# Performance work log

Hardware: AMD Instinct MI355X
Metric: run time of the kernel (lower is better)

The kernel has to match this reference:

```python
import jax, jax.numpy as jnp
import numpy as np
from jax.ops import segment_sum

N = 100000
E = 3200000
IN_DIM = 256
OUT_DIM = 64
LN_EPS = 1e-5
NEG_SLOPE = 0.01


def setup_inputs() -> dict:
    key = jax.random.key(0)
    k1, k2, k3, k4, k5 = jax.random.split(key, 5)
    x = jax.random.normal(k1, (N, IN_DIM), dtype=jnp.float32)
    edge_index = jax.random.randint(k2, (2, E), 0, N, dtype=jnp.int32)
    edge_weight = jax.random.uniform(k3, (E,), dtype=jnp.float32)
    # GCNConv params (glorot-ish scale) + LayerNorm params
    W = jax.random.normal(k4, (IN_DIM, OUT_DIM), dtype=jnp.float32) / np.sqrt(IN_DIM)
    b = jnp.zeros((OUT_DIM,), dtype=jnp.float32)
    gamma = jnp.ones((OUT_DIM,), dtype=jnp.float32)
    beta = jnp.zeros((OUT_DIM,), dtype=jnp.float32)
    return {"x": x, "edge_index": edge_index, "edge_weight": edge_weight,
            "W": W, "b": b, "gamma": gamma, "beta": beta}


def _gcn_forward(x, edge_index, edge_weight, W, b, gamma, beta):
    n = x.shape[0]
    # add self-loops with weight 1 (PyG GCNConv default)
    loops = jnp.arange(n, dtype=edge_index.dtype)
    src = jnp.concatenate([edge_index[0], loops])   # [E+N] message sources
    dst = jnp.concatenate([edge_index[1], loops])   # [E+N] aggregation targets
    ew = jnp.concatenate([edge_weight, jnp.ones((n,), dtype=edge_weight.dtype)])
    # symmetric normalization: deg computed on dst via weighted scatter
    deg = segment_sum(ew, dst, num_segments=n)                   # [N]
    dinv = jnp.where(deg > 0, jax.lax.rsqrt(deg), 0.0)           # deg^{-1/2}
    norm = dinv[src] * ew * dinv[dst]                            # [E+N]
    h = x @ W                                                    # [N, OUT]
    agg = segment_sum(h[src] * norm[:, None], dst, num_segments=n)  # [N, OUT]
    y = agg + b
    # leaky_relu then LayerNorm over last dim
    y = jnp.where(y >= 0, y, NEG_SLOPE * y)
    mu = jnp.mean(y, axis=-1, keepdims=True)
    var = jnp.mean(jnp.square(y - mu), axis=-1, keepdims=True)
    return (y - mu) * jax.lax.rsqrt(var + LN_EPS) * gamma + beta


def reference(x, edge_index, edge_weight, W, b, gamma, beta):
    return _gcn_forward(x, edge_index, edge_weight, W, b, gamma, beta)
```

## Files before the change

kernel.cpp:

```cpp
#include <hip/hip_runtime.h>

#define NN 100000
#define NE 3200000
#define OVCAP 65536

#define BINSZ 64
#define NBIN ((NN + BINSZ - 1) / BINSZ)
#define MAXPB 4096
#define SCAT_BLOCKS 512

struct OvEnt { int dst; int src; float ew; int pad; };


__global__ void k_zero(int* __restrict__ bincnt, int* __restrict__ ovcnt, int n) {
    int i = blockIdx.x * 256 + threadIdx.x;
    if (i < n) bincnt[i] = 0;
    if (i == 0) *ovcnt = 0;
}

__global__ __launch_bounds__(256) void k_binscatter(
    const int* __restrict__ src, const int* __restrict__ dst,
    const float* __restrict__ ew, int* __restrict__ bincnt,
    uint2* __restrict__ binbuf, int cap,
    OvEnt* __restrict__ ov, int* __restrict__ ovcnt, int e) {
    __shared__ int hist[NBIN];
    int t = threadIdx.x;
    int chunk = (e + gridDim.x - 1) / gridDim.x;
    int beg = blockIdx.x * chunk;
    int end = beg + chunk; if (end > e) end = e;
    for (int j = t; j < NBIN; j += 256) hist[j] = 0;
    __syncthreads();
    for (int i = beg + t; i < end; i += 256)
        atomicAdd(&hist[dst[i] >> 6], 1);
    __syncthreads();
    for (int j = t; j < NBIN; j += 256) {
        int c = hist[j];
        hist[j] = (c > 0) ? atomicAdd(&bincnt[j], c) : 0;
    }
    __syncthreads();
    for (int i = beg + t; i < end; i += 256) {
        int s = src[i], d = dst[i];
        float w = ew[i];
        int bin = d >> 6;
        int pos = atomicAdd(&hist[bin], 1);
        if (pos < cap) {
            unsigned key = (unsigned)s | ((unsigned)(d & 63) << 17);
            binbuf[(size_t)bin * cap + pos] = make_uint2(key, __float_as_uint(w));
        } else {
            int op = atomicAdd(ovcnt, 1);
            if (op < OVCAP) { OvEnt t2; t2.dst = d; t2.src = s; t2.ew = w; t2.pad = 0; ov[op] = t2; }
        }
    }
}

__global__ __launch_bounds__(256) void k_binsort(
    const int* __restrict__ bincnt, uint2* __restrict__ binbuf, int cap,
    const OvEnt* __restrict__ ov, const int* __restrict__ ovcnt,
    float* __restrict__ dinv, int* __restrict__ off, int* __restrict__ ncnt,
    int* __restrict__ binov, int n) {
    __shared__ float sdeg[BINSZ];
    __shared__ int hcnt[BINSZ];
    __shared__ int hoff[BINSZ];
    __shared__ int sov;
    __shared__ uint2 sbuf[MAXPB];
    int bin = blockIdx.x, t = threadIdx.x;
    if (t < BINSZ) { sdeg[t] = 0.f; hcnt[t] = 0; }
    if (t == 0) {
        int c = bincnt[bin];
        sov = (c > cap);
        binov[bin] = (c > cap);
    }
    __syncthreads();
    int cnt = bincnt[bin];
    int bc = cnt < cap ? cnt : cap;
    uint2* base = binbuf + (size_t)bin * cap;
    uint2 ent[16];
    int ne = 0;
#pragma unroll
    for (int p = 0; p < 16; p++) {
        int idx = t + p * 256;
        if (idx < bc) { ent[p] = base[idx]; ne = p + 1; }
    }
#pragma unroll
    for (int p = 0; p < 16; p++) {
        if (p < ne) {
            int dl = (int)((ent[p].x >> 17) & 63u);
            atomicAdd(&hcnt[dl], 1);
            atomicAdd(&sdeg[dl], __uint_as_float(ent[p].y));
        }
    }
    if (sov) {
        int on = *ovcnt; if (on > OVCAP) on = OVCAP;
        for (int j = t; j < on; j += 256) {
            OvEnt e2 = ov[j];
            if ((e2.dst >> 6) == bin) atomicAdd(&sdeg[e2.dst & 63], e2.ew);
        }
    }
    __syncthreads();
    if (t < 64) {
        int v = hcnt[t];
        int inc = v;
#pragma unroll
        for (int o2 = 1; o2 < 64; o2 <<= 1) {
            int u = __shfl_up(inc, o2, 64);
            if (t >= o2) inc += u;
        }
        int excl = inc - v;
        hoff[t] = excl;
        int g = bin * BINSZ + t;
        if (g < n) {
            dinv[g] = rsqrtf(1.0f + sdeg[t]);
            off[g] = bin * cap + excl;
            ncnt[g] = v;
        }
    }
    __syncthreads();
#pragma unroll
    for (int p = 0; p < 16; p++) {
        if (p < ne) {
            int dl = (int)((ent[p].x >> 17) & 63u);
            int pos = atomicAdd(&hoff[dl], 1);
            sbuf[pos] = ent[p];
        }
    }
    __syncthreads();
    for (int j = t; j < bc; j += 256) base[j] = sbuf[j];
}

__global__ __launch_bounds__(256) void k_norm(
    uint2* __restrict__ binbuf, const int* __restrict__ bincnt, int cap,
    const float* __restrict__ dinv, int n) {
    __shared__ float sd[BINSZ];
    int bin = blockIdx.x, t = threadIdx.x;
    if (t < BINSZ) {
        int g = bin * BINSZ + t;
        sd[t] = (g < n) ? dinv[g] : 0.f;
    }
    __syncthreads();
    int cnt = bincnt[bin];
    int bc = cnt < cap ? cnt : cap;
    uint2* base = binbuf + (size_t)bin * cap;
    for (int i = t; i < bc; i += 256) {
        uint2 v = base[i];
        int s = (int)(v.x & 0x1FFFFu);
        int dl = (int)((v.x >> 17) & 63u);
        float w = __uint_as_float(v.y) * dinv[s] * sd[dl];
        base[i] = make_uint2(v.x, __float_as_uint(w));
    }
}

__global__ __launch_bounds__(256) void k_gather_s(
    const float* __restrict__ h, const float* __restrict__ dinv,
    const int* __restrict__ binov,
    const int* __restrict__ off, const int* __restrict__ ncnt,
    const uint2* __restrict__ sorted,
    const OvEnt* __restrict__ ov, const int* __restrict__ ovcnt,
    const float* __restrict__ bias, const float* __restrict__ gamma,
    const float* __restrict__ beta, float* __restrict__ out, int n) {
    int lane = threadIdx.x & 63, wid = threadIdx.x >> 6;
    int node = blockIdx.x * 4 + wid;
    if (node >= n) return;
    float di = dinv[node];
    float acc = h[(size_t)node * 64 + lane] * di * di;
    int beg = off[node], c0 = ncnt[node];
    for (int j = 0; j < c0; j += 64) {
        int c = c0 - j; if (c > 64) c = 64;
        int s = 0; float w = 0.f;
        if (lane < c) {
            uint2 v = sorted[beg + j + lane];
            s = (int)(v.x & 0x1FFFFu);
            w = __uint_as_float(v.y);
        }
        int i2 = 0;
        for (; i2 + 16 <= c; i2 += 16) {
            float hv[16], wv[16];
#pragma unroll
            for (int q = 0; q < 16; q++) {
                int si = __shfl(s, i2 + q, 64);
                wv[q] = __shfl(w, i2 + q, 64);
                hv[q] = h[(size_t)si * 64 + lane];
            }
#pragma unroll
            for (int q = 0; q < 16; q++) acc += hv[q] * wv[q];
        }
        if (i2 < c) {
            float hv[16], wv[16];
            int rem = c - i2;
#pragma unroll
            for (int q = 0; q < 16; q++) {
                if (q < rem) {
                    int si = __shfl(s, i2 + q, 64);
                    wv[q] = __shfl(w, i2 + q, 64);
                    hv[q] = h[(size_t)si * 64 + lane];
                } else { wv[q] = 0.f; hv[q] = 0.f; }
            }
#pragma unroll
            for (int q = 0; q < 16; q++) acc += hv[q] * wv[q];
        }
    }
    if (binov[node >> 6]) {
        int on = *ovcnt; if (on > OVCAP) on = OVCAP;
        for (int j = 0; j < on; j++) {
            OvEnt ent = ov[j];
            if (ent.dst == node)
                acc += h[(size_t)ent.src * 64 + lane] * dinv[ent.src] * ent.ew * di;
        }
    }
    float y = acc + bias[lane];
    y = (y >= 0.f) ? y : 0.01f * y;
    float sum = y;
#pragma unroll
    for (int o = 32; o > 0; o >>= 1) sum += __shfl_xor(sum, o, 64);
    float mu = sum * (1.0f / 64.0f);
    float d = y - mu;
    float v = d * d;
#pragma unroll
    for (int o = 32; o > 0; o >>= 1) v += __shfl_xor(v, o, 64);
    v *= (1.0f / 64.0f);
    out[(size_t)node * 64 + lane] = d * rsqrtf(v + 1e-5f) * gamma[lane] + beta[lane];
}

#define GR 64
#define GKC 32
#define XS_STRIDE 36
__global__ __launch_bounds__(256) void k_gemm(const float* __restrict__ x,
                                              const float* __restrict__ W,
                                              float* __restrict__ h, int n) {
    __shared__ float xs[GR][XS_STRIDE];
    __shared__ float wsh[GKC][64];
    int t = threadIdx.x;
    int tx = t & 15;
    int ty = t >> 4;
    int rbase = blockIdx.x * GR;
    float acc[4][4];
#pragma unroll
    for (int i = 0; i < 4; i++)
#pragma unroll
        for (int j = 0; j < 4; j++) acc[i][j] = 0.0f;

    for (int k0 = 0; k0 < 256; k0 += GKC) {
        const float4* wsrc = (const float4*)(W + k0 * 64);
        float4* wdst = (float4*)(&wsh[0][0]);
        wdst[t] = wsrc[t];
        wdst[t + 256] = wsrc[t + 256];
#pragma unroll
        for (int p = 0; p < 2; p++) {
            int f4 = p * 256 + t;
            int r = f4 >> 3;
            int kq = (f4 & 7) << 2;
            int row = rbase + r;
            float4 val = make_float4(0.f, 0.f, 0.f, 0.f);
            if (row < n) val = *(const float4*)(x + (size_t)row * 256 + k0 + kq);
            *(float4*)(&xs[r][kq]) = val;
        }
        __syncthreads();
        int r0 = ty * 4, c0 = tx * 4;
#pragma unroll
        for (int kk = 0; kk < GKC; kk += 4) {
            float4 wv[4];
#pragma unroll
            for (int m = 0; m < 4; m++) wv[m] = *(const float4*)(&wsh[kk + m][c0]);
#pragma unroll
            for (int i = 0; i < 4; i++) {
                float4 xv = *(const float4*)(&xs[r0 + i][kk]);
                acc[i][0] += xv.x * wv[0].x + xv.y * wv[1].x + xv.z * wv[2].x + xv.w * wv[3].x;
                acc[i][1] += xv.x * wv[0].y + xv.y * wv[1].y + xv.z * wv[2].y + xv.w * wv[3].y;
                acc[i][2] += xv.x * wv[0].z + xv.y * wv[1].z + xv.z * wv[2].z + xv.w * wv[3].z;
                acc[i][3] += xv.x * wv[0].w + xv.y * wv[1].w + xv.z * wv[2].w + xv.w * wv[3].w;
            }
        }
        __syncthreads();
    }
    int r0 = ty * 4, c0 = tx * 4;
#pragma unroll
    for (int i = 0; i < 4; i++) {
        int row = rbase + r0 + i;
        if (row < n) {
            float4 v = make_float4(acc[i][0], acc[i][1], acc[i][2], acc[i][3]);
            *(float4*)(h + (size_t)row * 64 + c0) = v;
        }
    }
}


__global__ void k_init(float* __restrict__ deg, int* __restrict__ cnt, int n) {
    int i = blockIdx.x * 256 + threadIdx.x;
    if (i < n) { deg[i] = 1.0f; cnt[i] = 0; }
}

__global__ void k_deg(const int* __restrict__ dst, const float* __restrict__ ew,
                      float* __restrict__ deg, int* __restrict__ cnt, int e) {
    int i = blockIdx.x * 256 + threadIdx.x;
    if (i < e) {
        int d = dst[i];
        atomicAdd(&deg[d], ew[i]);
        atomicAdd(&cnt[d], 1);
    }
}

#define SCAN_T 256
#define SCAN_E 8
__global__ void k_scan_blocks(const int* __restrict__ cnt, int* __restrict__ off,
                              int* __restrict__ bsum, int n) {
    __shared__ int sdata[SCAN_T];
    int base = blockIdx.x * (SCAN_T * SCAN_E);
    int t = threadIdx.x;
    int v[SCAN_E];
    int local = 0;
    int idx0 = base + t * SCAN_E;
#pragma unroll
    for (int i = 0; i < SCAN_E; i++) {
        int idx = idx0 + i;
        int c = (idx < n) ? cnt[idx] : 0;
        v[i] = local;
        local += c;
    }
    sdata[t] = local;
    __syncthreads();
    for (int o = 1; o < SCAN_T; o <<= 1) {
        int x = 0;
        if (t >= o) x = sdata[t - o];
        __syncthreads();
        sdata[t] += x;
        __syncthreads();
    }
    int excl = sdata[t] - local;
#pragma unroll
    for (int i = 0; i < SCAN_E; i++) {
        int idx = idx0 + i;
        if (idx < n) off[idx] = excl + v[i];
    }
    if (t == SCAN_T - 1) bsum[blockIdx.x] = sdata[t];
}

__global__ void k_scan_bsums(int* __restrict__ bsum, int nb) {
    int t = threadIdx.x;
    int v = (t < nb) ? bsum[t] : 0;
    int orig = v;
#pragma unroll
    for (int o = 1; o < 64; o <<= 1) {
        int u = __shfl_up(v, o, 64);
        if (t >= o) v += u;
    }
    if (t < nb) bsum[t] = v - orig;
}

__global__ void k_finalize(int* __restrict__ off, const int* __restrict__ bsum,
                           int* __restrict__ cursor, float* __restrict__ deg,
                           int n, int total) {
    int i = blockIdx.x * 256 + threadIdx.x;
    if (i < n) {
        int o = off[i] + bsum[i >> 11];
        off[i] = o;
        cursor[i] = o;
        deg[i] = rsqrtf(deg[i]);
    }
    if (i == 0) off[n] = total;
}

__global__ void k_scatter(const int* __restrict__ src, const int* __restrict__ dst,
                          const float* __restrict__ ew, const float* __restrict__ dinv,
                          int* __restrict__ cursor, int* __restrict__ ssrc,
                          float* __restrict__ snorm, int e) {
    int i = blockIdx.x * 256 + threadIdx.x;
    if (i < e) {
        int s = src[i], d = dst[i];
        float nm = dinv[s] * ew[i] * dinv[d];
        int pos = atomicAdd(&cursor[d], 1);
        ssrc[pos] = s;
        snorm[pos] = nm;
    }
}

__global__ __launch_bounds__(256) void k_gather(
    const float* __restrict__ h, const float* __restrict__ dinv,
    const int* __restrict__ off, const int* __restrict__ ssrc,
    const float* __restrict__ snorm, const float* __restrict__ bias,
    const float* __restrict__ gamma, const float* __restrict__ beta,
    float* __restrict__ out, int n) {
    int lane = threadIdx.x & 63;
    int wid = threadIdx.x >> 6;
    int node = blockIdx.x * 4 + wid;
    if (node >= n) return;
    float di = dinv[node];
    float acc = h[(size_t)node * 64 + lane] * di * di;
    int beg = off[node], end = off[node + 1];
    for (int j = beg; j < end; j += 64) {
        int cnt = end - j;
        if (cnt > 64) cnt = 64;
        int s = 0;
        float w = 0.f;
        if (lane < cnt) { s = ssrc[j + lane]; w = snorm[j + lane]; }
        for (int i2 = 0; i2 < cnt; i2++) {
            int si = __shfl(s, i2, 64);
            float wi = __shfl(w, i2, 64);
            acc += h[(size_t)si * 64 + lane] * wi;
        }
    }
    float y = acc + bias[lane];
    y = (y >= 0.f) ? y : 0.01f * y;
    float sum = y;
#pragma unroll
    for (int o = 32; o > 0; o >>= 1) sum += __shfl_xor(sum, o, 64);
    float mu = sum * (1.0f / 64.0f);
    float d = y - mu;
    float v = d * d;
#pragma unroll
    for (int o = 32; o > 0; o >>= 1) v += __shfl_xor(v, o, 64);
    v *= (1.0f / 64.0f);
    out[(size_t)node * 64 + lane] = d * rsqrtf(v + 1e-5f) * gamma[lane] + beta[lane];
}


extern "C" void kernel_launch(void* const* d_in, const int* in_sizes, int n_in,
                              void* d_out, int out_size, void* d_ws, size_t ws_size,
                              hipStream_t stream) {
    const float* x = (const float*)d_in[0];
    const int* ei = (const int*)d_in[1];
    const float* ew = (const float*)d_in[2];
    const float* W = (const float*)d_in[3];
    const float* b = (const float*)d_in[4];
    const float* gamma = (const float*)d_in[5];
    const float* beta = (const float*)d_in[6];
    float* out = (float*)d_out;

    const int n = NN, e = NE;
    const int* src = ei;
    const int* dst = ei + e;

    char* ws = (char*)d_ws;
    size_t o = 0;
    auto alloc = [&](size_t bytes) -> char* {
        char* r = ws + o;
        o = (o + bytes + 255) & ~(size_t)255;
        return r;
    };
    auto pad = [](size_t bytes) -> size_t { return (bytes + 255) & ~(size_t)255; };

    int nb_n = (n + 255) / 256;
    int nb_e = (e + 255) / 256;
    int nb_gemm = (n + GR - 1) / GR;
    int nb_w = (n + 3) / 4;

    size_t fixed = 0;
    fixed += pad((size_t)NBIN * 4);
    fixed += 256;
    fixed += pad((size_t)OVCAP * 16);
    fixed += pad((size_t)n * 4);
    fixed += pad((size_t)n * 4);
    fixed += pad((size_t)n * 4);
    fixed += pad((size_t)NBIN * 4);
    fixed += pad((size_t)n * 64 * 4);

    int cap = 0;
    if (ws_size >= fixed + pad((size_t)NBIN * 4096 * 8) + 8192) cap = 4096;
    else if (ws_size >= fixed + pad((size_t)NBIN * 3072 * 8) + 8192) cap = 3072;

    if (cap > 0) {
        int* bincnt = (int*)alloc((size_t)NBIN * 4);
        int* ovcnt = (int*)alloc(4);
        OvEnt* ov = (OvEnt*)alloc((size_t)OVCAP * 16);
        float* dinv = (float*)alloc((size_t)n * 4);
        int* off = (int*)alloc((size_t)n * 4);
        int* ncnt = (int*)alloc((size_t)n * 4);
        int* binov = (int*)alloc((size_t)NBIN * 4);
        float* h = (float*)alloc((size_t)n * 64 * 4);
        uint2* binbuf = (uint2*)alloc((size_t)NBIN * cap * 8);

        int nb_z = (NBIN + 255) / 256;
        k_zero<<<nb_z, 256, 0, stream>>>(bincnt, ovcnt, NBIN);
        k_binscatter<<<SCAT_BLOCKS, 256, 0, stream>>>(src, dst, ew, bincnt, binbuf, cap,
                                                      ov, ovcnt, e);
        k_binsort<<<NBIN, 256, 0, stream>>>(bincnt, binbuf, cap, ov, ovcnt,
                                            dinv, off, ncnt, binov, n);
        k_norm<<<NBIN, 256, 0, stream>>>(binbuf, bincnt, cap, dinv, n);
        k_gemm<<<nb_gemm, 256, 0, stream>>>(x, W, h, n);
        k_gather_s<<<nb_w, 256, 0, stream>>>(h, dinv, binov, off, ncnt, binbuf,
                                             ov, ovcnt, b, gamma, beta, out, n);
    } else {
        float* deg = (float*)alloc((size_t)n * 4);
        int* cnt = (int*)alloc((size_t)n * 4);
        int* off = (int*)alloc((size_t)(n + 1) * 4);
        int* cursor = (int*)alloc((size_t)n * 4);
        int* bsum = (int*)alloc(64 * 4);
        float* h = (float*)alloc((size_t)n * 64 * 4);
        int* ssrc = (int*)alloc((size_t)e * 4);
        float* snorm = (float*)alloc((size_t)e * 4);
        int nb_scan = (n + SCAN_T * SCAN_E - 1) / (SCAN_T * SCAN_E);

        k_init<<<nb_n, 256, 0, stream>>>(deg, cnt, n);
        k_deg<<<nb_e, 256, 0, stream>>>(dst, ew, deg, cnt, e);
        k_scan_blocks<<<nb_scan, SCAN_T, 0, stream>>>(cnt, off, bsum, n);
        k_scan_bsums<<<1, 64, 0, stream>>>(bsum, nb_scan);
        k_finalize<<<nb_n, 256, 0, stream>>>(off, bsum, cursor, deg, n, e);
        k_scatter<<<nb_e, 256, 0, stream>>>(src, dst, ew, deg, cursor, ssrc, snorm, e);
        k_gemm<<<nb_gemm, 256, 0, stream>>>(x, W, h, n);
        k_gather<<<nb_w, 256, 0, stream>>>(h, deg, off, ssrc, snorm, b, gamma, beta, out, n);
    }
}
```

Baseline: 486.9 us.

## Fuse bin sort, edge normalization and gather into one per-bin kernel

```diff
diff --git a/kernel.cpp b/kernel.cpp
--- a/kernel.cpp
+++ b/kernel.cpp
@@ -53,43 +53,22 @@
     }
 }
 
-__global__ __launch_bounds__(256) void k_binsort(
-    const int* __restrict__ bincnt, uint2* __restrict__ binbuf, int cap,
+__global__ __launch_bounds__(256) void k_deg2(
+    const int* __restrict__ bincnt, const uint2* __restrict__ binbuf, int cap,
     const OvEnt* __restrict__ ov, const int* __restrict__ ovcnt,
-    float* __restrict__ dinv, int* __restrict__ off, int* __restrict__ ncnt,
-    int* __restrict__ binov, int n) {
+    float* __restrict__ dinv, int n) {
     __shared__ float sdeg[BINSZ];
-    __shared__ int hcnt[BINSZ];
-    __shared__ int hoff[BINSZ];
-    __shared__ int sov;
-    __shared__ uint2 sbuf[MAXPB];
     int bin = blockIdx.x, t = threadIdx.x;
-    if (t < BINSZ) { sdeg[t] = 0.f; hcnt[t] = 0; }
-    if (t == 0) {
-        int c = bincnt[bin];
-        sov = (c > cap);
-        binov[bin] = (c > cap);
-    }
+    if (t < BINSZ) sdeg[t] = 0.f;
     __syncthreads();
     int cnt = bincnt[bin];
     int bc = cnt < cap ? cnt : cap;
-    uint2* base = binbuf + (size_t)bin * cap;
-    uint2 ent[16];
-    int ne = 0;
-#pragma unroll
-    for (int p = 0; p < 16; p++) {
-        int idx = t + p * 256;
-        if (idx < bc) { ent[p] = base[idx]; ne = p + 1; }
-    }
-#pragma unroll
-    for (int p = 0; p < 16; p++) {
-        if (p < ne) {
-            int dl = (int)((ent[p].x >> 17) & 63u);
-            atomicAdd(&hcnt[dl], 1);
-            atomicAdd(&sdeg[dl], __uint_as_float(ent[p].y));
-        }
-    }
-    if (sov) {
+    const uint2* base = binbuf + (size_t)bin * cap;
+    for (int i = t; i < bc; i += 256) {
+        uint2 v = base[i];
+        atomicAdd(&sdeg[(v.x >> 17) & 63u], __uint_as_float(v.y));
+    }
+    if (cnt > cap) {
         int on = *ovcnt; if (on > OVCAP) on = OVCAP;
         for (int j = t; j < on; j += 256) {
             OvEnt e2 = ov[j];
@@ -97,9 +76,49 @@
         }
     }
     __syncthreads();
+    if (t < BINSZ) {
+        int g = bin * BINSZ + t;
+        if (g < n) dinv[g] = rsqrtf(1.0f + sdeg[t]);
+    }
+}
+
+__global__ __launch_bounds__(256) void k_sortgather(
+    const float* __restrict__ h, const float* __restrict__ dinv,
+    const int* __restrict__ bincnt, const uint2* __restrict__ binbuf, int cap,
+    const OvEnt* __restrict__ ov, const int* __restrict__ ovcnt,
+    const float* __restrict__ bias, const float* __restrict__ gamma,
+    const float* __restrict__ beta, float* __restrict__ out, int n) {
+    __shared__ uint2 sbuf[MAXPB];
+    __shared__ float sd[BINSZ];
+    __shared__ int hcnt[BINSZ];
+    __shared__ int hoff[BINSZ];
+    __shared__ int noff[BINSZ];
+    int bin = blockIdx.x, t = threadIdx.x;
+    int lane = t & 63, wid = t >> 6;
+
+    if (t < BINSZ) {
+        hcnt[t] = 0;
+        int g = bin * BINSZ + t;
+        sd[t] = (g < n) ? dinv[g] : 0.f;
+    }
+    __syncthreads();
+    int cnt = bincnt[bin];
+    int bc = cnt < cap ? cnt : cap;
+    const uint2* base = binbuf + (size_t)bin * cap;
+
+    uint2 ent[16];
+    int ne = 0;
+#pragma unroll
+    for (int p = 0; p < 16; p++) {
+        int idx = t + p * 256;
+        if (idx < bc) { ent[p] = base[idx]; ne = p + 1; }
+    }
+#pragma unroll
+    for (int p = 0; p < 16; p++)
+        if (p < ne) atomicAdd(&hcnt[(int)((ent[p].x >> 17) & 63u)], 1);
+    __syncthreads();
     if (t < 64) {
-        int v = hcnt[t];
-        int inc = v;
+        int v = hcnt[t], inc = v;
 #pragma unroll
         for (int o2 = 1; o2 < 64; o2 <<= 1) {
             int u = __shfl_up(inc, o2, 64);
@@ -107,12 +126,7 @@
         }
         int excl = inc - v;
         hoff[t] = excl;
-        int g = bin * BINSZ + t;
-        if (g < n) {
-            dinv[g] = rsqrtf(1.0f + sdeg[t]);
-            off[g] = bin * cap + excl;
-            ncnt[g] = v;
-        }
+        noff[t] = excl;
     }
     __syncthreads();
 #pragma unroll
@@ -124,100 +138,71 @@
         }
     }
     __syncthreads();
-    for (int j = t; j < bc; j += 256) base[j] = sbuf[j];
-}
-
-__global__ __launch_bounds__(256) void k_norm(
-    uint2* __restrict__ binbuf, const int* __restrict__ bincnt, int cap,
-    const float* __restrict__ dinv, int n) {
-    __shared__ float sd[BINSZ];
-    int bin = blockIdx.x, t = threadIdx.x;
-    if (t < BINSZ) {
-        int g = bin * BINSZ + t;
-        sd[t] = (g < n) ? dinv[g] : 0.f;
-    }
-    __syncthreads();
-    int cnt = bincnt[bin];
-    int bc = cnt < cap ? cnt : cap;
-    uint2* base = binbuf + (size_t)bin * cap;
-    for (int i = t; i < bc; i += 256) {
-        uint2 v = base[i];
-        int s = (int)(v.x & 0x1FFFFu);
-        int dl = (int)((v.x >> 17) & 63u);
-        float w = __uint_as_float(v.y) * dinv[s] * sd[dl];
-        base[i] = make_uint2(v.x, __float_as_uint(w));
-    }
-}
-
-__global__ __launch_bounds__(256) void k_gather_s(
-    const float* __restrict__ h, const float* __restrict__ dinv,
-    const int* __restrict__ binov,
-    const int* __restrict__ off, const int* __restrict__ ncnt,
-    const uint2* __restrict__ sorted,
-    const OvEnt* __restrict__ ov, const int* __restrict__ ovcnt,
-    const float* __restrict__ bias, const float* __restrict__ gamma,
-    const float* __restrict__ beta, float* __restrict__ out, int n) {
-    int lane = threadIdx.x & 63, wid = threadIdx.x >> 6;
-    int node = blockIdx.x * 4 + wid;
-    if (node >= n) return;
-    float di = dinv[node];
-    float acc = h[(size_t)node * 64 + lane] * di * di;
-    int beg = off[node], c0 = ncnt[node];
-    for (int j = 0; j < c0; j += 64) {
-        int c = c0 - j; if (c > 64) c = 64;
-        int s = 0; float w = 0.f;
-        if (lane < c) {
-            uint2 v = sorted[beg + j + lane];
-            s = (int)(v.x & 0x1FFFFu);
-            w = __uint_as_float(v.y);
-        }
-        int i2 = 0;
-        for (; i2 + 16 <= c; i2 += 16) {
-            float hv[16], wv[16];
-#pragma unroll
-            for (int q = 0; q < 16; q++) {
-                int si = __shfl(s, i2 + q, 64);
-                wv[q] = __shfl(w, i2 + q, 64);
-                hv[q] = h[(size_t)si * 64 + lane];
+
+    int sov = (cnt > cap);
+    float bi = bias[lane], ga = gamma[lane], be = beta[lane];
+    for (int dl = wid; dl < BINSZ; dl += 4) {
+        int g = bin * BINSZ + dl;
+        if (g >= n) break;
+        float di = sd[dl];
+        float acc = h[(size_t)g * 64 + lane] * di * di;
+        int start = noff[dl], c0 = hcnt[dl];
+        for (int j = 0; j < c0; j += 64) {
+            int c = c0 - j; if (c > 64) c = 64;
+            int s = 0; float w = 0.f;
+            if (lane < c) {
+                uint2 v = sbuf[start + j + lane];
+                s = (int)(v.x & 0x1FFFFu);
+                w = __uint_as_float(v.y) * dinv[s] * di;
             }
-#pragma unroll
-            for (int q = 0; q < 16; q++) acc += hv[q] * wv[q];
-        }
-        if (i2 < c) {
-            float hv[16], wv[16];
-            int rem = c - i2;
-#pragma unroll
-            for (int q = 0; q < 16; q++) {
-                if (q < rem) {
+            int i2 = 0;
+            for (; i2 + 16 <= c; i2 += 16) {
+                float hv[16], wv[16];
+#pragma unroll
+                for (int q = 0; q < 16; q++) {
                     int si = __shfl(s, i2 + q, 64);
                     wv[q] = __shfl(w, i2 + q, 64);
                     hv[q] = h[(size_t)si * 64 + lane];
-                } else { wv[q] = 0.f; hv[q] = 0.f; }
+                }
+#pragma unroll
+                for (int q = 0; q < 16; q++) acc += hv[q] * wv[q];
             }
-#pragma unroll
-            for (int q = 0; q < 16; q++) acc += hv[q] * wv[q];
-        }
-    }
-    if (binov[node >> 6]) {
-        int on = *ovcnt; if (on > OVCAP) on = OVCAP;
-        for (int j = 0; j < on; j++) {
-            OvEnt ent = ov[j];
-            if (ent.dst == node)
-                acc += h[(size_t)ent.src * 64 + lane] * dinv[ent.src] * ent.ew * di;
-        }
-    }
-    float y = acc + bias[lane];
-    y = (y >= 0.f) ? y : 0.01f * y;
-    float sum = y;
-#pragma unroll
-    for (int o = 32; o > 0; o >>= 1) sum += __shfl_xor(sum, o, 64);
-    float mu = sum * (1.0f / 64.0f);
-    float d = y - mu;
-    float v = d * d;
-#pragma unroll
-    for (int o = 32; o > 0; o >>= 1) v += __shfl_xor(v, o, 64);
-    v *= (1.0f / 64.0f);
-    out[(size_t)node * 64 + lane] = d * rsqrtf(v + 1e-5f) * gamma[lane] + beta[lane];
+            if (i2 < c) {
+                float hv[16], wv[16];
+                int rem = c - i2;
+#pragma unroll
+                for (int q = 0; q < 16; q++) {
+                    if (q < rem) {
+                        int si = __shfl(s, i2 + q, 64);
+                        wv[q] = __shfl(w, i2 + q, 64);
+                        hv[q] = h[(size_t)si * 64 + lane];
+                    } else { wv[q] = 0.f; hv[q] = 0.f; }
+                }
+#pragma unroll
+                for (int q = 0; q < 16; q++) acc += hv[q] * wv[q];
+            }
+        }
+        if (sov) {
+            int on = *ovcnt; if (on > OVCAP) on = OVCAP;
+            for (int j2 = 0; j2 < on; j2++) {
+                OvEnt e2 = ov[j2];
+                if (e2.dst == g)
+                    acc += h[(size_t)e2.src * 64 + lane] * dinv[e2.src] * e2.ew * di;
+            }
+        }
+        float y = acc + bi;
+        y = (y >= 0.f) ? y : 0.01f * y;
+        float sum = y;
+#pragma unroll
+        for (int o = 32; o > 0; o >>= 1) sum += __shfl_xor(sum, o, 64);
+        float mu = sum * (1.0f / 64.0f);
+        float d = y - mu;
+        float v = d * d;
+#pragma unroll
+        for (int o = 32; o > 0; o >>= 1) v += __shfl_xor(v, o, 64);
+        v *= (1.0f / 64.0f);
+        out[(size_t)g * 64 + lane] = d * rsqrtf(v + 1e-5f) * ga + be;
+    }
 }
 
 #define GR 64
@@ -440,16 +425,12 @@
     int nb_n = (n + 255) / 256;
     int nb_e = (e + 255) / 256;
     int nb_gemm = (n + GR - 1) / GR;
-    int nb_w = (n + 3) / 4;
 
     size_t fixed = 0;
     fixed += pad((size_t)NBIN * 4);
     fixed += 256;
     fixed += pad((size_t)OVCAP * 16);
     fixed += pad((size_t)n * 4);
-    fixed += pad((size_t)n * 4);
-    fixed += pad((size_t)n * 4);
-    fixed += pad((size_t)NBIN * 4);
     fixed += pad((size_t)n * 64 * 4);
 
     int cap = 0;
@@ -461,9 +442,6 @@
         int* ovcnt = (int*)alloc(4);
         OvEnt* ov = (OvEnt*)alloc((size_t)OVCAP * 16);
         float* dinv = (float*)alloc((size_t)n * 4);
-        int* off = (int*)alloc((size_t)n * 4);
-        int* ncnt = (int*)alloc((size_t)n * 4);
-        int* binov = (int*)alloc((size_t)NBIN * 4);
         float* h = (float*)alloc((size_t)n * 64 * 4);
         uint2* binbuf = (uint2*)alloc((size_t)NBIN * cap * 8);
 
@@ -471,12 +449,10 @@
         k_zero<<<nb_z, 256, 0, stream>>>(bincnt, ovcnt, NBIN);
         k_binscatter<<<SCAT_BLOCKS, 256, 0, stream>>>(src, dst, ew, bincnt, binbuf, cap,
                                                       ov, ovcnt, e);
-        k_binsort<<<NBIN, 256, 0, stream>>>(bincnt, binbuf, cap, ov, ovcnt,
-                                            dinv, off, ncnt, binov, n);
-        k_norm<<<NBIN, 256, 0, stream>>>(binbuf, bincnt, cap, dinv, n);
+        k_deg2<<<NBIN, 256, 0, stream>>>(bincnt, binbuf, cap, ov, ovcnt, dinv, n);
         k_gemm<<<nb_gemm, 256, 0, stream>>>(x, W, h, n);
-        k_gather_s<<<nb_w, 256, 0, stream>>>(h, dinv, binov, off, ncnt, binbuf,
-                                             ov, ovcnt, b, gamma, beta, out, n);
+        k_sortgather<<<NBIN, 256, 0, stream>>>(h, dinv, bincnt, binbuf, cap,
+                                               ov, ovcnt, b, gamma, beta, out, n);
     } else {
         float* deg = (float*)alloc((size_t)n * 4);
         int* cnt = (int*)alloc((size_t)n * 4);
@@ -487,6 +463,7 @@
         int* ssrc = (int*)alloc((size_t)e * 4);
         float* snorm = (float*)alloc((size_t)e * 4);
         int nb_scan = (n + SCAN_T * SCAN_E - 1) / (SCAN_T * SCAN_E);
+        int nb_w = (n + 3) / 4;
 
         k_init<<<nb_n, 256, 0, stream>>>(deg, cnt, n);
         k_deg<<<nb_e, 256, 0, stream>>>(dst, ew, deg, cnt, e);
```

New measurement: 468.9 us. 1.04x faster.
